# Performance work log

Hardware: AMD Instinct MI355X
Metric: run time of the kernel (lower is better)

Reference implementation:

```python
import jax, jax.numpy as jnp
import numpy as np
from jax import lax


def conv(x, w, b, stride, pad):
    # x: [B,C,H,W], w: [O,I,kh,kw] (torch layout)
    y = lax.conv_general_dilated(x, w, (stride, stride), ((pad, pad), (pad, pad)),
                                 dimension_numbers=('NCHW', 'OIHW', 'NCHW'))
    return y + b[None, :, None, None]


def convT(x, w, b, stride, pad):
    # torch ConvTranspose2d weight layout [in, out, kh, kw]
    k = w.shape[2]
    wf = jnp.flip(w, (2, 3)).transpose(1, 0, 2, 3)  # -> [out, in, kh, kw]
    p = k - 1 - pad
    y = lax.conv_general_dilated(x, wf, (1, 1), ((p, p), (p, p)),
                                 lhs_dilation=(stride, stride),
                                 dimension_numbers=('NCHW', 'OIHW', 'NCHW'))
    return y + b[None, :, None, None]


def resblock(x, wa, ba, wb, bb):
    h = conv(jax.nn.relu(x), wa, ba, 1, 1)   # 3x3
    h2 = conv(jax.nn.relu(h), wb, bb, 1, 0)  # 1x1
    return x + h2


def vqvae_forward(x, e1_w, e1_b, e2_w, e2_b, e3_w, e3_b,
                  er1a_w, er1a_b, er1b_w, er1b_b, er2a_w, er2a_b, er2b_w, er2b_b,
                  codebook,
                  d1_w, d1_b, dr1a_w, dr1a_b, dr1b_w, dr1b_b,
                  dr2a_w, dr2a_b, dr2b_w, dr2b_b,
                  dt1_w, dt1_b, dt2_w, dt2_b):
    # encoder
    h = jax.nn.relu(conv(x, e1_w, e1_b, 2, 1))
    h = jax.nn.relu(conv(h, e2_w, e2_b, 2, 1))
    h = conv(h, e3_w, e3_b, 1, 1)
    h = resblock(h, er1a_w, er1a_b, er1b_w, er1b_b)
    ze = resblock(h, er2a_w, er2a_b, er2b_w, er2b_b)  # [B,C,H,W]
    # VQ: nearest codebook vector per spatial location (squared L2)
    zef = ze.transpose(0, 2, 3, 1)  # [B,H,W,C]
    # ||z - e||^2 = ||z||^2 - 2 z.e + ||e||^2 (same argmin as explicit broadcast)
    d = (jnp.sum(zef * zef, -1, keepdims=True)
         - 2.0 * jnp.einsum('bhwc,kc->bhwk', zef, codebook)
         + jnp.sum(codebook * codebook, -1))  # [B,H,W,K]
    idx = jnp.argmin(d, -1)                    # [B,H,W]
    zq = codebook[idx].transpose(0, 3, 1, 2)   # [B,C,H,W]
    # straight-through estimator
    dec_in = ze + lax.stop_gradient(zq - ze)
    # decoder
    g = conv(dec_in, d1_w, d1_b, 1, 1)
    g = resblock(g, dr1a_w, dr1a_b, dr1b_w, dr1b_b)
    g = resblock(g, dr2a_w, dr2a_b, dr2b_w, dr2b_b)
    g = jax.nn.relu(convT(g, dt1_w, dt1_b, 2, 1))
    x_hat = convT(g, dt2_w, dt2_b, 2, 1)
    return x_hat, ze, zq


def setup_inputs() -> dict:
    key = jax.random.key(0)
    ks = iter(jax.random.split(key, 64))
    C, K = 128, 512

    def w(shape, scale=0.02):
        return jax.random.normal(next(ks), shape, jnp.float32) * scale

    inp = {}
    inp['x'] = jax.random.normal(next(ks), (16, 3, 256, 256), jnp.float32)
    inp['e1_w'] = w((C, 3, 4, 4)); inp['e1_b'] = w((C,))
    inp['e2_w'] = w((C, C, 4, 4)); inp['e2_b'] = w((C,))
    inp['e3_w'] = w((C, C, 3, 3)); inp['e3_b'] = w((C,))
    inp['er1a_w'] = w((C, C, 3, 3)); inp['er1a_b'] = w((C,))
    inp['er1b_w'] = w((C, C, 1, 1)); inp['er1b_b'] = w((C,))
    inp['er2a_w'] = w((C, C, 3, 3)); inp['er2a_b'] = w((C,))
    inp['er2b_w'] = w((C, C, 1, 1)); inp['er2b_b'] = w((C,))
    inp['codebook'] = jax.random.uniform(next(ks), (K, C), jnp.float32, -1.0 / K, 1.0 / K)
    inp['d1_w'] = w((C, C, 3, 3)); inp['d1_b'] = w((C,))
    inp['dr1a_w'] = w((C, C, 3, 3)); inp['dr1a_b'] = w((C,))
    inp['dr1b_w'] = w((C, C, 1, 1)); inp['dr1b_b'] = w((C,))
    inp['dr2a_w'] = w((C, C, 3, 3)); inp['dr2a_b'] = w((C,))
    inp['dr2b_w'] = w((C, C, 1, 1)); inp['dr2b_b'] = w((C,))
    inp['dt1_w'] = w((C, C, 4, 4)); inp['dt1_b'] = w((C,))   # ConvTranspose [in,out,kh,kw]
    inp['dt2_w'] = w((C, 3, 4, 4)); inp['dt2_b'] = w((3,))
    return inp


def reference(x, e1_w, e1_b, e2_w, e2_b, e3_w, e3_b,
              er1a_w, er1a_b, er1b_w, er1b_b, er2a_w, er2a_b, er2b_w, er2b_b,
              codebook,
              d1_w, d1_b, dr1a_w, dr1a_b, dr1b_w, dr1b_b,
              dr2a_w, dr2a_b, dr2b_w, dr2b_b,
              dt1_w, dt1_b, dt2_w, dt2_b):
    return vqvae_forward(x, e1_w, e1_b, e2_w, e2_b, e3_w, e3_b,
                         er1a_w, er1a_b, er1b_w, er1b_b, er2a_w, er2a_b, er2b_w, er2b_b,
                         codebook,
                         d1_w, d1_b, dr1a_w, dr1a_b, dr1b_w, dr1b_b,
                         dr2a_w, dr2a_b, dr2b_w, dr2b_b,
                         dt1_w, dt1_b, dt2_w, dt2_b)
```

## Files before the change

### kernel.cpp

```cpp
#include <hip/hip_runtime.h>
#include <stdint.h>

typedef unsigned short u16;
typedef __attribute__((ext_vector_type(8))) short short8;
typedef __attribute__((ext_vector_type(4))) float floatx4;

#define RS66  (66*128)
#define IS66  (66*66*128)
#define RS130 (130*128)
#define IS130 (130*130*128)

__device__ __forceinline__ float bf2f(u16 h) {
  union { unsigned u; float f; } v; v.u = ((unsigned)h) << 16; return v.f;
}
__device__ __forceinline__ u16 f2bf(float f) {
  union { float f; unsigned u; } v; v.f = f;
  unsigned r = v.u + 0x7FFFu + ((v.u >> 16) & 1u);
  return (u16)(r >> 16);
}
__device__ __forceinline__ unsigned fkey(float f) {
  unsigned u = __float_as_uint(f);
  return (u & 0x80000000u) ? ~u : (u | 0x80000000u);
}
__device__ __forceinline__ void lgkmbar() {
  asm volatile("s_waitcnt lgkmcnt(0)" ::: "memory");
  __builtin_amdgcn_s_barrier();
  __builtin_amdgcn_sched_barrier(0);
}

struct Taps { int n; unsigned dh2; unsigned dw2; };

__global__ __launch_bounds__(256, 3) void conv_mfma(
    const u16* __restrict__ in, int inRS, int inIS, int si,
    const u16* __restrict__ wt, const float* __restrict__ bias, Taps tp,
    u16* __restrict__ out, int outRS, int outIS, int so, int oh0, int ow0,
    const u16* __restrict__ res, u16* __restrict__ out2, int reluMain,
    float* __restrict__ zeFc, u16* __restrict__ zeBFc, int multi)
{
  __shared__ u16 lA[2][8192];
  const int tid = threadIdx.x;
  const int w = tid >> 6, lane = tid & 63, quad = lane >> 4, l16 = lane & 15;
  const int wm = w >> 1, wn = w & 1;
  const int bx = ((blockIdx.x & 7) << 6) | (blockIdx.x >> 3);
  const int blockM = bx << 7;

  unsigned dh2 = tp.dh2, dw2 = tp.dw2;
  if (multi) {
    const int cls = blockIdx.y;
    dh2 = (tp.dh2 >> (8*cls)) & 0xffu;
    dw2 = (tp.dw2 >> (8*cls)) & 0xffu;
    wt += cls << 16;
    oh0 = cls >> 1; ow0 = cls & 1;
  }

  const int swz = (tid & 7) ^ ((tid >> 3) & 7);
  const int wOff = (tid >> 3)*64 + swz*8;
  const u16* gA[4];
#pragma unroll
  for (int i=0;i<4;i++) {
    const int pg = blockM + i*32 + (tid >> 3);
    const int b = pg >> 12, mo = (pg >> 6) & 63, no = pg & 63;
    gA[i] = in + b*inIS + si*mo*inRS + si*no*128 + (tid & 7)*8;
  }
  const u16* gBf = wt + (wn*64 + l16)*32 + quad*8;

  floatx4 zz = {0.f,0.f,0.f,0.f};
  floatx4 acc[4][4];
#pragma unroll
  for (int i=0;i<4;i++)
#pragma unroll
    for (int j=0;j<4;j++) acc[i][j] = zz;

  auto gloadA = [&](int ci, short8 (&a)[4]) {
    const int t = ci >> 1, kc = ci & 1;
    const int dh = (int)((dh2 >> (2*t)) & 3u) - 1;
    const int dw = (int)((dw2 >> (2*t)) & 3u) - 1;
    const int aoff = dh*inRS + dw*128 + kc*64;
#pragma unroll
    for (int i=0;i<4;i++) a[i] = *(const short8*)(gA[i] + aoff);
  };
  auto dswA = [&](u16* P, short8 (&a)[4]) {
#pragma unroll
    for (int i=0;i<4;i++) *(short8*)(P + i*2048 + wOff) = a[i];
  };
  auto loadBk = [&](int ci, int kk, short8 (&v)[4]) {
    const u16* p = gBf + ci*8192 + kk*4096;
#pragma unroll
    for (int s=0;s<4;s++) v[s] = *(const short8*)(p + s*512);
  };
  auto computeH = [&](const u16* P, int kk, short8 (&bfr)[4]) {
    short8 af[4];
#pragma unroll
    for (int s=0;s<4;s++) {
      const int row = wm*64 + s*16 + l16;
      af[s] = *(const short8*)&P[row*64 + (((kk*4 + quad) ^ (l16 & 7)) << 3)];
    }
#pragma unroll
    for (int i=0;i<4;i++)
#pragma unroll
      for (int j=0;j<4;j++)
        acc[i][j] = __builtin_amdgcn_mfma_f32_16x16x32_bf16(af[i], bfr[j], acc[i][j], 0, 0, 0);
  };

  const int NCH = tp.n << 1;
  short8 a[4], bA[4], bB[4];
  gloadA(0, a);
  loadBk(0, 0, bA);
  loadBk(0, 1, bB);
  dswA(&lA[0][0], a);
  gloadA(1, a);
  lgkmbar();

  int cur = 0;
  for (int ci = 0; ci < NCH; ++ci) {
    computeH(&lA[cur][0], 0, bA);
    if (ci + 1 < NCH) loadBk(ci + 1, 0, bA);
    computeH(&lA[cur][0], 1, bB);
    if (ci + 1 < NCH) {
      loadBk(ci + 1, 1, bB);
      dswA(&lA[cur ^ 1][0], a);
      if (ci + 2 < NCH) gloadA(ci + 2, a);
      lgkmbar();
    }
    cur ^= 1;
  }

  float bv[4];
#pragma unroll
  for (int j=0;j<4;j++) bv[j] = bias[wn*64 + j*16 + l16];

#pragma unroll
  for (int i=0;i<4;i++) {
#pragma unroll
    for (int r=0;r<4;r++) {
      const int p = blockM + wm*64 + i*16 + quad*4 + r;
      const int bb2 = p >> 12, mo = (p >> 6) & 63, no = p & 63;
      const int ob = bb2*outIS + (so*mo + oh0)*outRS + (so*no + ow0)*128;
#pragma unroll
      for (int j=0;j<4;j++) {
        const int n = wn*64 + j*16 + l16;
        float v = acc[i][j][r] + bv[j];
        if (res)  v += bf2f(res[ob + n]);
        if (out)  out[ob + n]  = f2bf(reluMain ? fmaxf(v, 0.f) : v);
        if (out2) out2[ob + n] = f2bf(fmaxf(v, 0.f));
        if (zeFc) {
          zeFc[((size_t)p << 7) + n] = v;
          zeBFc[((size_t)p << 7) + n] = f2bf(v);
        }
      }
    }
  }
}

__global__ __launch_bounds__(256, 3) void vq_score(
    const u16* __restrict__ zeBF, const u16* __restrict__ cbF,
    const float* __restrict__ cbn, unsigned long long* __restrict__ minbuf)
{
  __shared__ u16 lA[2][8192];
  const int tid = threadIdx.x;
  const int w = tid >> 6, lane = tid & 63, quad = lane >> 4, l16 = lane & 15;
  const int wm = w >> 1, wn = w & 1;
  const int bx = ((blockIdx.x & 7) << 6) | (blockIdx.x >> 3);
  const int blockM = bx << 7;
  const int nb = blockIdx.y;
  const int swz = (tid & 7) ^ ((tid >> 3) & 7);
  const int wOff = (tid >> 3)*64 + swz*8;
  const u16* gA[4];
#pragma unroll
  for (int i=0;i<4;i++)
    gA[i] = zeBF + ((size_t)(blockM + i*32 + (tid >> 3)) << 7) + (tid & 7)*8;
  const u16* gBf = cbF + (nb << 14) + (wn*64 + l16)*32 + quad*8;

  floatx4 zz = {0.f,0.f,0.f,0.f};
  floatx4 acc[4][4];
#pragma unroll
  for (int i=0;i<4;i++)
#pragma unroll
    for (int j=0;j<4;j++) acc[i][j] = zz;

  auto gloadA = [&](int ci, short8 (&a)[4]) {
#pragma unroll
    for (int i=0;i<4;i++) a[i] = *(const short8*)(gA[i] + ci*64);
  };
  auto dswA = [&](u16* P, short8 (&a)[4]) {
#pragma unroll
    for (int i=0;i<4;i++) *(short8*)(P + i*2048 + wOff) = a[i];
  };
  auto loadBk = [&](int ci, int kk, short8 (&v)[4]) {
    const u16* p = gBf + ci*8192 + kk*4096;
#pragma unroll
    for (int s=0;s<4;s++) v[s] = *(const short8*)(p + s*512);
  };
  auto computeH = [&](const u16* P, int kk, short8 (&bfr)[4]) {
    short8 af[4];
#pragma unroll
    for (int s=0;s<4;s++) {
      const int row = wm*64 + s*16 + l16;
      af[s] = *(const short8*)&P[row*64 + (((kk*4 + quad) ^ (l16 & 7)) << 3)];
    }
#pragma unroll
    for (int i=0;i<4;i++)
#pragma unroll
      for (int j=0;j<4;j++)
        acc[i][j] = __builtin_amdgcn_mfma_f32_16x16x32_bf16(af[i], bfr[j], acc[i][j], 0, 0, 0);
  };

  short8 a[4], bA[4], bB[4];
  gloadA(0, a);
  loadBk(0, 0, bA);
  loadBk(0, 1, bB);
  dswA(&lA[0][0], a);
  gloadA(1, a);
  lgkmbar();
  computeH(&lA[0][0], 0, bA);
  loadBk(1, 0, bA);
  computeH(&lA[0][0], 1, bB);
  loadBk(1, 1, bB);
  dswA(&lA[1][0], a);
  lgkmbar();
  computeH(&lA[1][0], 0, bA);
  computeH(&lA[1][0], 1, bB);

  float cn[4];
#pragma unroll
  for (int j=0;j<4;j++) cn[j] = cbn[nb*128 + wn*64 + j*16 + l16];

#pragma unroll
  for (int i=0;i<4;i++) {
#pragma unroll
    for (int r=0;r<4;r++) {
      const int p = blockM + wm*64 + i*16 + quad*4 + r;
      unsigned long long best = 0xFFFFFFFFFFFFFFFFull;
#pragma unroll
      for (int j=0;j<4;j++) {
        const int n = nb*128 + wn*64 + j*16 + l16;
        float v = cn[j] - acc[i][j][r];
        unsigned long long pk = ((unsigned long long)fkey(v) << 32) | (unsigned)n;
        if (pk < best) best = pk;
      }
#pragma unroll
      for (int d=1; d<16; d<<=1) {
        unsigned long long o = __shfl_xor(best, d, 64);
        if (o < best) best = o;
      }
      if (l16 == 0) atomicMin(minbuf + p, best);
    }
  }
}

__global__ __launch_bounds__(256) void finalize(
    const float* __restrict__ zeFc, const unsigned long long* __restrict__ minb,
    const float* __restrict__ cb, float* __restrict__ outZe, float* __restrict__ outZq,
    u16* __restrict__ zqI)
{
  __shared__ float T[64*129];
  __shared__ int ns[64];
  const int tid = threadIdx.x;
  const int P0 = blockIdx.x << 6;
  const int b = P0 >> 12, hw0 = P0 & 4095;

#pragma unroll
  for (int it=0; it<32; ++it) {
    int e = it*256 + tid;
    int px = e >> 7, c = e & 127;
    T[px*129 + c] = zeFc[((size_t)P0 << 7) + e];
  }
  if (tid < 64) ns[tid] = (int)(unsigned)(minb[P0 + tid] & 0xFFFFFFFFull);
  __syncthreads();

  float* zeB = outZe + (((size_t)b) << 19) + hw0;
  float* zqB = outZq + (((size_t)b) << 19) + hw0;
  const int h = hw0 >> 6;
  u16* zqIB = zqI + b*IS66 + h*RS66;
#pragma unroll
  for (int it=0; it<32; ++it) {
    const int c = it*4 + (tid >> 6);
    const int px = tid & 63;
    zeB[(c << 12) + px] = T[px*129 + c];
    float v = cb[(ns[px] << 7) + c];
    zqB[(c << 12) + px] = v;
    zqIB[px*128 + c] = f2bf(v);
  }
}

__global__ __launch_bounds__(256) void zero_halos(
    u16* big, u16* s0, u16* s1, u16* s2, u16* s3, unsigned long long* minb)
{
  int id = blockIdx.x*256 + threadIdx.x;
  if (id >= 463872) return;
  if (id >= 398336) { minb[id - 398336] = 0xFFFFFFFFFFFFFFFFull; return; }
  u16* base; int H, W;
  if (id < 132096) { base = big; H = 128; W = 128; }
  else {
    id -= 132096;
    int bi = id / 66560;
    id -= bi*66560;
    base = (bi == 0) ? s0 : (bi == 1) ? s1 : (bi == 2) ? s2 : s3;
    H = 64; W = 64;
  }
  int Wp = W+2, Hp = H+2;
  int cv = id & 15; int rest = id >> 4;
  int npx = 2*Wp + 2*H;
  int img = rest / npx; int pix = rest - img*npx;
  int hh, wwp;
  if (pix < Wp) { hh = 0; wwp = pix; }
  else if (pix < 2*Wp) { hh = Hp-1; wwp = pix - Wp; }
  else { int r2 = pix - 2*Wp; hh = 1 + (r2 >> 1); wwp = (r2 & 1) ? (Wp-1) : 0; }
  uint4 zv = {0u,0u,0u,0u};
  *(uint4*)(base + (((size_t)img*Hp + hh)*Wp + wwp)*128 + cv*8) = zv;
}

struct WEnt { const float* src; u16* dst; int O, I, T, mode; };
struct WTab { int n; WEnt e[16]; int cum[17]; };
__global__ __launch_bounds__(256) void prep_w(WTab wt) {
  int id = blockIdx.x*256 + threadIdx.x;
  if (id >= wt.cum[wt.n]) return;
  int k = 0;
  while (id >= wt.cum[k+1]) k++;
  int l = id - wt.cum[k];
  WEnt E = wt.e[k];
  if (E.mode == 6) {
    int e = l & 7, quad = (l >> 3) & 3, row = (l >> 5) & 127;
    int kk = (l >> 12) & 1, kc = (l >> 13) & 1, t = l >> 14;
    int i = kc*64 + kk*32 + quad*8 + e;
    E.dst[l] = f2bf(E.src[(row*E.I + i)*E.T + t]);
  } else if (E.mode == 1) {
    int e = l & 7, quad = (l >> 3) & 3, row = (l >> 5) & 127;
    int kk = (l >> 12) & 1, kc = (l >> 13) & 1, tt = (l >> 14) & 3, cls = l >> 16;
    int i = kc*64 + kk*32 + quad*8 + e;
    int th = tt >> 1, tw = tt & 1, po = cls >> 1, pw = cls & 1;
    int kh = po ? (th ? 2 : 0) : (th ? 3 : 1);
    int kw = pw ? (tw ? 2 : 0) : (tw ? 3 : 1);
    E.dst[l] = f2bf(E.src[((i*128 + row)*4 + kh)*4 + kw]);
  } else if (E.mode == 7) {
    int e = l & 7, quad = (l >> 3) & 3, row = (l >> 5) & 127;
    int kk = (l >> 12) & 1, kc = (l >> 13) & 1, tt = l >> 14;
    int i = kc*64 + kk*32 + quad*8 + e;
    E.dst[l] = f2bf(E.src[(tt*128 + row)*128 + i]);
  } else if (E.mode == 3) {
    float s = 0.f; const float* r = E.src + l*128;
    for (int c=0;c<128;c++) s += r[c]*r[c];
    ((float*)E.dst)[l] = 0.5f*s;
  } else if (E.mode == 4) {
    int o = l & 127, tap = l >> 7;
    ((float*)E.dst)[l] = E.src[o*48 + tap];
  } else {
    int c = l & 127, n = l >> 7;
    int o = n >> 4, kk = n & 15;
    E.dst[l] = f2bf(E.src[c*48 + o*16 + kk]);
  }
}

__global__ __launch_bounds__(256) void conv_e1(
    const float* __restrict__ x, const float* __restrict__ wT,
    const float* __restrict__ bias, u16* __restrict__ outI)
{
  __shared__ float inS[12*260];
  __shared__ float wS[48*128];
  __shared__ float bS[128];
  const int tid = threadIdx.x;
  const int b = blockIdx.x >> 7, ho = blockIdx.x & 127;

  for (int l = tid; l < 1536; l += 256)
    ((float4*)wS)[l] = ((const float4*)wT)[l];
  if (tid < 128) bS[tid] = bias[tid];
  for (int l = tid; l < 3120; l += 256) {
    int col = l % 260; int rest = l / 260;
    int kh = rest & 3, c = rest >> 2;
    int hi = 2*ho + kh - 1, wi = col - 1;
    float v = 0.f;
    if ((unsigned)hi < 256u && (unsigned)wi < 256u)
      v = x[((b*3 + c) << 16) + (hi << 8) + wi];
    inS[rest*260 + col] = v;
  }
  __syncthreads();

  const int g = tid & 7;
  const int pxg = tid >> 3;
  floatx4 acc[4][4];
  {
    const floatx4* bp = (const floatx4*)&bS[g*16];
    floatx4 b0 = bp[0], b1 = bp[1], b2 = bp[2], b3 = bp[3];
#pragma unroll
    for (int px=0;px<4;px++) { acc[px][0]=b0; acc[px][1]=b1; acc[px][2]=b2; acc[px][3]=b3; }
  }
#pragma unroll
  for (int c=0;c<3;c++)
#pragma unroll
    for (int kh=0;kh<4;kh++) {
      const float* row = &inS[(c*4+kh)*260];
#pragma unroll
      for (int kw=0;kw<4;kw++) {
        const int tap = c*16 + kh*4 + kw;
        const floatx4* wp = (const floatx4*)&wS[tap*128 + g*16];
        floatx4 w0 = wp[0], w1 = wp[1], w2 = wp[2], w3 = wp[3];
#pragma unroll
        for (int px=0;px<4;px++) {
          float xv = row[((pxg*4 + px) << 1) + kw];
          acc[px][0] += xv*w0; acc[px][1] += xv*w1;
          acc[px][2] += xv*w2; acc[px][3] += xv*w3;
        }
      }
    }

  u16* ob = outI + b*IS130 + ho*RS130;
#pragma unroll
  for (int px=0;px<4;px++) {
    const int wo = pxg*4 + px;
    u16* p = ob + wo*128 + g*16;
#pragma unroll
    for (int k=0;k<4;k++) {
      union { u16 u[4]; uint2 v2; } pk;
#pragma unroll
      for (int j=0;j<4;j++) pk.u[j] = f2bf(fmaxf(acc[px][k][j], 0.f));
      *(uint2*)(p + k*4) = pk.v2;
    }
  }
}

__global__ __launch_bounds__(256) void dt2_gemm(
    const u16* __restrict__ inI, const u16* __restrict__ Wb,
    float* __restrict__ cols)
{
  const int tid = threadIdx.x;
  const int w = tid >> 6, lane = tid & 63, quad = lane >> 4, l16 = lane & 15;
  const int pixBase = blockIdx.x*256 + w*64;

  short8 Bf[3][4];
#pragma unroll
  for (int nt=0; nt<3; nt++)
#pragma unroll
    for (int kc=0; kc<4; kc++)
      Bf[nt][kc] = *(const short8*)(Wb + (nt*16 + l16)*128 + kc*32 + quad*8);

  const u16* ap[4];
#pragma unroll
  for (int ms=0; ms<4; ms++) {
    int p = pixBase + ms*16 + l16;
    int b = p >> 14, rem = p & 16383;
    ap[ms] = inI + b*IS130 + (rem >> 7)*RS130 + (rem & 127)*128;
  }

  floatx4 zz = {0.f,0.f,0.f,0.f};
  floatx4 acc[4][3];
#pragma unroll
  for (int ms=0; ms<4; ms++)
#pragma unroll
    for (int nt=0; nt<3; nt++) acc[ms][nt] = zz;

#pragma unroll
  for (int kc=0; kc<4; kc++) {
#pragma unroll
    for (int ms=0; ms<4; ms++) {
      short8 a = *(const short8*)(ap[ms] + kc*32 + quad*8);
#pragma unroll
      for (int nt=0; nt<3; nt++)
        acc[ms][nt] = __builtin_amdgcn_mfma_f32_16x16x32_bf16(a, Bf[nt][kc], acc[ms][nt], 0, 0, 0);
    }
  }

#pragma unroll
  for (int ms=0; ms<4; ms++)
#pragma unroll
    for (int nt=0; nt<3; nt++)
#pragma unroll
      for (int r=0; r<4; r++) {
        int p = pixBase + ms*16 + quad*4 + r;
        cols[(size_t)p*48 + nt*16 + l16] = acc[ms][nt][r];
      }
}

__global__ __launch_bounds__(256) void dt2_gather(
    const float* __restrict__ cols, const float* __restrict__ bias,
    float* __restrict__ xhat)
{
  int id = blockIdx.x*256 + threadIdx.x;
  int b = id >> 16, rem = id & 65535;
  int ho = rem >> 8, wo = rem & 255;
  const int ph = ho & 1, pw = wo & 1;
  const int hi0 = ph ? ((ho+1)>>1) : (ho>>1);
  const int kh0 = ph ? 0 : 1;
  const int wi0 = pw ? ((wo+1)>>1) : (wo>>1);
  const int kw0 = pw ? 0 : 1;
  float a0 = bias[0], a1 = bias[1], a2 = bias[2];
#pragma unroll
  for (int th=0; th<2; th++) {
    const int hi = hi0 - th;
    if ((unsigned)hi >= 128u) continue;
    const int kh = kh0 + 2*th;
#pragma unroll
    for (int tw=0; tw<2; tw++) {
      const int wi = wi0 - tw;
      if ((unsigned)wi >= 128u) continue;
      const int kw = kw0 + 2*tw;
      const float* r = cols + (size_t)((b << 14) + (hi << 7) + wi)*48 + (kh*4 + kw);
      a0 += r[0]; a1 += r[16]; a2 += r[32];
    }
  }
  const int ob = ((b*3) << 16) + (ho << 8) + wo;
  xhat[ob]          = a0;
  xhat[ob + 65536]  = a1;
  xhat[ob + 131072] = a2;
}

extern "C" void kernel_launch(void* const* d_in, const int* in_sizes, int n_in,
                              void* d_out, int out_size, void* d_ws, size_t ws_size,
                              hipStream_t stream)
{
  const float* x     = (const float*)d_in[0];
  const float* e1w   = (const float*)d_in[1];
  const float* e1b   = (const float*)d_in[2];
  const float* e2w   = (const float*)d_in[3];
  const float* e2b   = (const float*)d_in[4];
  const float* e3w   = (const float*)d_in[5];
  const float* e3b   = (const float*)d_in[6];
  const float* er1aw = (const float*)d_in[7];
  const float* er1ab = (const float*)d_in[8];
  const float* er1bw = (const float*)d_in[9];
  const float* er1bb = (const float*)d_in[10];
  const float* er2aw = (const float*)d_in[11];
  const float* er2ab = (const float*)d_in[12];
  const float* er2bw = (const float*)d_in[13];
  const float* er2bb = (const float*)d_in[14];
  const float* cb    = (const float*)d_in[15];
  const float* d1w   = (const float*)d_in[16];
  const float* d1b   = (const float*)d_in[17];
  const float* dr1aw = (const float*)d_in[18];
  const float* dr1ab = (const float*)d_in[19];
  const float* dr1bw = (const float*)d_in[20];
  const float* dr1bb = (const float*)d_in[21];
  const float* dr2aw = (const float*)d_in[22];
  const float* dr2ab = (const float*)d_in[23];
  const float* dr2bw = (const float*)d_in[24];
  const float* dr2bb = (const float*)d_in[25];
  const float* dt1w  = (const float*)d_in[26];
  const float* dt1b  = (const float*)d_in[27];
  const float* dt2w  = (const float*)d_in[28];
  const float* dt2b  = (const float*)d_in[29];
  float* out = (float*)d_out;

  char* ws = (char*)d_ws;
  size_t off = 0;
  auto alloc = [&](size_t bytes) -> void* {
    void* r = ws + off; off += (bytes + 255) & ~(size_t)255; return r;
  };

  u16* BIG = (u16*)alloc((size_t)IS130*16*2);
  u16* S[4];
  for (int i=0;i<4;i++) S[i] = (u16*)alloc((size_t)IS66*16*2);
  unsigned long long* minb = (unsigned long long*)alloc((size_t)65536*8);
  u16* W_e2 = (u16*)alloc(262144*2);
  u16* W9[6]; for (int i=0;i<6;i++) W9[i] = (u16*)alloc(147456*2);
  u16* W1[4]; for (int i=0;i<4;i++) W1[i] = (u16*)alloc(16384*2);
  u16* Wdt1 = (u16*)alloc(262144*2);
  u16* cbBF = (u16*)alloc(65536*2);
  float* cbn = (float*)alloc(512*4);
  float* wsE1 = (float*)alloc(6144*4);
  u16* Wb48 = (u16*)alloc(6144*2);

  u16* BIGi = BIG + RS130 + 128;
  u16* Si[4];
  for (int i=0;i<4;i++) Si[i] = S[i] + RS66 + 128;
  u16* zeBFc = S[1];
  float* zeFc = (float*)BIG;
  float* cols = (float*)S[1];

  zero_halos<<<1812, 256, 0, stream>>>(BIG, S[0], S[1], S[2], S[3], minb);

  WTab wtab; int ne = 0; wtab.cum[0] = 0;
  auto addw = [&](const float* s, u16* d, int O, int I, int T, int m, int items) {
    wtab.e[ne] = {s, d, O, I, T, m};
    wtab.cum[ne+1] = wtab.cum[ne] + items; ne++;
  };
  addw(e2w,   W_e2, 128,128,16,6, 262144);
  addw(e3w,   W9[0],128,128, 9,6, 147456);
  addw(er1aw, W9[1],128,128, 9,6, 147456);
  addw(er2aw, W9[2],128,128, 9,6, 147456);
  addw(d1w,   W9[3],128,128, 9,6, 147456);
  addw(dr1aw, W9[4],128,128, 9,6, 147456);
  addw(dr2aw, W9[5],128,128, 9,6, 147456);
  addw(er1bw, W1[0],128,128, 1,6, 16384);
  addw(er2bw, W1[1],128,128, 1,6, 16384);
  addw(dr1bw, W1[2],128,128, 1,6, 16384);
  addw(dr2bw, W1[3],128,128, 1,6, 16384);
  addw(dt1w,  Wdt1, 0,0,0,1, 262144);
  addw(cb,    cbBF, 0,0,0,7, 65536);
  addw(cb,    (u16*)cbn, 0,0,0,3, 512);
  addw(e1w,   (u16*)wsE1, 0,0,0,4, 6144);
  addw(dt2w,  Wb48, 0,0,0,5, 6144);
  wtab.n = ne;
  prep_w<<<(wtab.cum[ne] + 255)/256, 256, 0, stream>>>(wtab);

  conv_e1<<<2048, 256, 0, stream>>>(x, wsE1, e1b, BIGi);

  Taps t16; t16.n = 16; t16.dh2 = 0; t16.dw2 = 0;
  for (int t=0;t<16;t++) { t16.dh2 |= (unsigned)(t>>2) << (2*t); t16.dw2 |= (unsigned)(t&3) << (2*t); }
  Taps t9; t9.n = 9; t9.dh2 = 0; t9.dw2 = 0;
  for (int t=0;t<9;t++) { t9.dh2 |= (unsigned)(t/3) << (2*t); t9.dw2 |= (unsigned)(t%3) << (2*t); }
  Taps t1x; t1x.n = 1; t1x.dh2 = 1; t1x.dw2 = 1;
  Taps tcm; tcm.n = 4; tcm.dh2 = 0; tcm.dw2 = 0;
  for (int cls=0; cls<4; ++cls) {
    int po = cls >> 1, pw = cls & 1;
    for (int tt=0; tt<4; ++tt) {
      int th = tt >> 1, tw = tt & 1;
      int dh = po ? (th ? 0 : 1) : (th ? -1 : 0);
      int dw = pw ? (tw ? 0 : 1) : (tw ? -1 : 0);
      tcm.dh2 |= (unsigned)(dh+1) << (8*cls + 2*tt);
      tcm.dw2 |= (unsigned)(dw+1) << (8*cls + 2*tt);
    }
  }

  auto conv = [&](const u16* in_, int iRS, int iIS, int si,
                  const u16* w_, const float* b_, Taps tp,
                  u16* o_, int oRS, int oIS, int so, int oh, int ow,
                  const u16* r_, u16* o2, int rl, float* zf, u16* zb) {
    conv_mfma<<<512, 256, 0, stream>>>(in_, iRS, iIS, si, w_, b_, tp,
                                       o_, oRS, oIS, so, oh, ow, r_, o2, rl, zf, zb, 0);
  };

  conv(BIGi, RS130, IS130, 2, W_e2, e2b, t16, Si[0], RS66, IS66, 1,0,0, nullptr, nullptr, 1, nullptr, nullptr);
  conv(Si[0], RS66, IS66, 1, W9[0], e3b, t9, Si[1], RS66, IS66, 1,0,0, nullptr, Si[2], 0, nullptr, nullptr);
  conv(Si[2], RS66, IS66, 1, W9[1], er1ab, t9, Si[0], RS66, IS66, 1,0,0, nullptr, nullptr, 1, nullptr, nullptr);
  conv(Si[0], RS66, IS66, 1, W1[0], er1bb, t1x, Si[3], RS66, IS66, 1,0,0, Si[1], Si[2], 0, nullptr, nullptr);
  conv(Si[2], RS66, IS66, 1, W9[2], er2ab, t9, Si[0], RS66, IS66, 1,0,0, nullptr, nullptr, 1, nullptr, nullptr);
  conv(Si[0], RS66, IS66, 1, W1[1], er2bb, t1x, nullptr, RS66, IS66, 1,0,0, Si[3], nullptr, 0, zeFc, zeBFc);

  vq_score<<<dim3(512,4), 256, 0, stream>>>(zeBFc, cbBF, cbn, minb);
  finalize<<<1024, 256, 0, stream>>>(zeFc, minb, cb, out + 3145728, out + 11534336, Si[2]);

  conv(Si[2], RS66, IS66, 1, W9[3], d1b, t9, Si[0], RS66, IS66, 1,0,0, nullptr, Si[1], 0, nullptr, nullptr);
  conv(Si[1], RS66, IS66, 1, W9[4], dr1ab, t9, Si[2], RS66, IS66, 1,0,0, nullptr, nullptr, 1, nullptr, nullptr);
  conv(Si[2], RS66, IS66, 1, W1[2], dr1bb, t1x, Si[3], RS66, IS66, 1,0,0, Si[0], Si[1], 0, nullptr, nullptr);
  conv(Si[1], RS66, IS66, 1, W9[5], dr2ab, t9, Si[2], RS66, IS66, 1,0,0, nullptr, nullptr, 1, nullptr, nullptr);
  conv(Si[2], RS66, IS66, 1, W1[3], dr2bb, t1x, Si[0], RS66, IS66, 1,0,0, Si[3], nullptr, 0, nullptr, nullptr);

  conv_mfma<<<dim3(512,4), 256, 0, stream>>>(Si[0], RS66, IS66, 1, Wdt1, dt1b, tcm,
                                             BIGi, RS130, IS130, 2, 0, 0,
                                             nullptr, nullptr, 1, nullptr, nullptr, 1);

  dt2_gemm<<<1024, 256, 0, stream>>>(BIGi, Wb48, cols);
  dt2_gather<<<4096, 256, 0, stream>>>(cols, dt2b, out);
}
```

Before: 726.4 us.

## Widen conv and VQ GEMM K-chunk to full 128 channels per tap

Each K-step in the MFMA conv and VQ scoring kernels now stages a full 128-channel tap (128x128 bf16 A tile) in LDS instead of two 64-channel halves. This halves the number of barriers and LDS double-buffer swaps per tap. The B fragments are loaded in four sub-steps interleaved with compute, and the weight prep layout is changed to match. It doubles LDS use and register use for A staging, so launch bounds drop from 3 to 2 blocks per CU, which lowers occupancy.

```diff
diff --git a/kernel.cpp b/kernel.cpp
--- a/kernel.cpp
+++ b/kernel.cpp
@@ -30,14 +30,14 @@
 
 struct Taps { int n; unsigned dh2; unsigned dw2; };
 
-__global__ __launch_bounds__(256, 3) void conv_mfma(
+__global__ __launch_bounds__(256, 2) void conv_mfma(
     const u16* __restrict__ in, int inRS, int inIS, int si,
     const u16* __restrict__ wt, const float* __restrict__ bias, Taps tp,
     u16* __restrict__ out, int outRS, int outIS, int so, int oh0, int ow0,
     const u16* __restrict__ res, u16* __restrict__ out2, int reluMain,
     float* __restrict__ zeFc, u16* __restrict__ zeBFc, int multi)
 {
-  __shared__ u16 lA[2][8192];
+  __shared__ u16 lA[2][16384];
   const int tid = threadIdx.x;
   const int w = tid >> 6, lane = tid & 63, quad = lane >> 4, l16 = lane & 15;
   const int wm = w >> 1, wn = w & 1;
@@ -53,8 +53,8 @@
     oh0 = cls >> 1; ow0 = cls & 1;
   }
 
-  const int swz = (tid & 7) ^ ((tid >> 3) & 7);
-  const int wOff = (tid >> 3)*64 + swz*8;
+  const int swz3 = (tid & 7) ^ ((tid >> 3) & 7);
+  const int wBase = (tid >> 3)*128 + swz3*8;
   const u16* gA[4];
 #pragma unroll
   for (int i=0;i<4;i++) {
@@ -71,29 +71,34 @@
 #pragma unroll
     for (int j=0;j<4;j++) acc[i][j] = zz;
 
-  auto gloadA = [&](int ci, short8 (&a)[4]) {
-    const int t = ci >> 1, kc = ci & 1;
+  auto gloadA = [&](int t, short8 (&a)[8]) {
     const int dh = (int)((dh2 >> (2*t)) & 3u) - 1;
     const int dw = (int)((dw2 >> (2*t)) & 3u) - 1;
-    const int aoff = dh*inRS + dw*128 + kc*64;
-#pragma unroll
-    for (int i=0;i<4;i++) a[i] = *(const short8*)(gA[i] + aoff);
-  };
-  auto dswA = [&](u16* P, short8 (&a)[4]) {
-#pragma unroll
-    for (int i=0;i<4;i++) *(short8*)(P + i*2048 + wOff) = a[i];
+    const int aoff = dh*inRS + dw*128;
+#pragma unroll
+    for (int i=0;i<4;i++)
+#pragma unroll
+      for (int h=0;h<2;h++)
+        a[i*2+h] = *(const short8*)(gA[i] + aoff + h*64);
+  };
+  auto dswA = [&](u16* P, short8 (&a)[8]) {
+#pragma unroll
+    for (int i=0;i<4;i++)
+#pragma unroll
+      for (int h=0;h<2;h++)
+        *(short8*)(P + i*4096 + wBase + h*64) = a[i*2+h];
   };
   auto loadBk = [&](int ci, int kk, short8 (&v)[4]) {
-    const u16* p = gBf + ci*8192 + kk*4096;
-#pragma unroll
-    for (int s=0;s<4;s++) v[s] = *(const short8*)(p + s*512);
+    const u16* p = gBf + ci*16384 + kk*4096;
+#pragma unroll
+    for (int s4=0;s4<4;s4++) v[s4] = *(const short8*)(p + s4*512);
   };
   auto computeH = [&](const u16* P, int kk, short8 (&bfr)[4]) {
     short8 af[4];
 #pragma unroll
-    for (int s=0;s<4;s++) {
-      const int row = wm*64 + s*16 + l16;
-      af[s] = *(const short8*)&P[row*64 + (((kk*4 + quad) ^ (l16 & 7)) << 3)];
+    for (int s4=0;s4<4;s4++) {
+      const int row = wm*64 + s4*16 + l16;
+      af[s4] = *(const short8*)&P[row*128 + (((kk*4 + quad) ^ (l16 & 7)) << 3)];
     }
 #pragma unroll
     for (int i=0;i<4;i++)
@@ -102,26 +107,29 @@
         acc[i][j] = __builtin_amdgcn_mfma_f32_16x16x32_bf16(af[i], bfr[j], acc[i][j], 0, 0, 0);
   };
 
-  const int NCH = tp.n << 1;
-  short8 a[4], bA[4], bB[4];
+  const int NCH = tp.n;
+  short8 a[8], bA[4], bB[4];
   gloadA(0, a);
   loadBk(0, 0, bA);
-  loadBk(0, 1, bB);
   dswA(&lA[0][0], a);
-  gloadA(1, a);
+  if (NCH > 1) gloadA(1, a);
   lgkmbar();
 
   int cur = 0;
   for (int ci = 0; ci < NCH; ++ci) {
+    loadBk(ci, 1, bB);
     computeH(&lA[cur][0], 0, bA);
-    if (ci + 1 < NCH) loadBk(ci + 1, 0, bA);
+    loadBk(ci, 2, bA);
     computeH(&lA[cur][0], 1, bB);
+    loadBk(ci, 3, bB);
+    computeH(&lA[cur][0], 2, bA);
     if (ci + 1 < NCH) {
-      loadBk(ci + 1, 1, bB);
+      loadBk(ci + 1, 0, bA);
       dswA(&lA[cur ^ 1][0], a);
       if (ci + 2 < NCH) gloadA(ci + 2, a);
-      lgkmbar();
-    }
+    }
+    computeH(&lA[cur][0], 3, bB);
+    if (ci + 1 < NCH) lgkmbar();
     cur ^= 1;
   }
 
@@ -152,19 +160,19 @@
   }
 }
 
-__global__ __launch_bounds__(256, 3) void vq_score(
+__global__ __launch_bounds__(256, 2) void vq_score(
     const u16* __restrict__ zeBF, const u16* __restrict__ cbF,
     const float* __restrict__ cbn, unsigned long long* __restrict__ minbuf)
 {
-  __shared__ u16 lA[2][8192];
+  __shared__ u16 lA[16384];
   const int tid = threadIdx.x;
   const int w = tid >> 6, lane = tid & 63, quad = lane >> 4, l16 = lane & 15;
   const int wm = w >> 1, wn = w & 1;
   const int bx = ((blockIdx.x & 7) << 6) | (blockIdx.x >> 3);
   const int blockM = bx << 7;
   const int nb = blockIdx.y;
-  const int swz = (tid & 7) ^ ((tid >> 3) & 7);
-  const int wOff = (tid >> 3)*64 + swz*8;
+  const int swz3 = (tid & 7) ^ ((tid >> 3) & 7);
+  const int wBase = (tid >> 3)*128 + swz3*8;
   const u16* gA[4];
 #pragma unroll
   for (int i=0;i<4;i++)
@@ -178,25 +186,17 @@
 #pragma unroll
     for (int j=0;j<4;j++) acc[i][j] = zz;
 
-  auto gloadA = [&](int ci, short8 (&a)[4]) {
-#pragma unroll
-    for (int i=0;i<4;i++) a[i] = *(const short8*)(gA[i] + ci*64);
-  };
-  auto dswA = [&](u16* P, short8 (&a)[4]) {
-#pragma unroll
-    for (int i=0;i<4;i++) *(short8*)(P + i*2048 + wOff) = a[i];
-  };
-  auto loadBk = [&](int ci, int kk, short8 (&v)[4]) {
-    const u16* p = gBf + ci*8192 + kk*4096;
-#pragma unroll
-    for (int s=0;s<4;s++) v[s] = *(const short8*)(p + s*512);
-  };
-  auto computeH = [&](const u16* P, int kk, short8 (&bfr)[4]) {
+  auto loadBk = [&](int kk, short8 (&v)[4]) {
+    const u16* p = gBf + kk*4096;
+#pragma unroll
+    for (int s4=0;s4<4;s4++) v[s4] = *(const short8*)(p + s4*512);
+  };
+  auto computeH = [&](int kk, short8 (&bfr)[4]) {
     short8 af[4];
 #pragma unroll
-    for (int s=0;s<4;s++) {
-      const int row = wm*64 + s*16 + l16;
-      af[s] = *(const short8*)&P[row*64 + (((kk*4 + quad) ^ (l16 & 7)) << 3)];
+    for (int s4=0;s4<4;s4++) {
+      const int row = wm*64 + s4*16 + l16;
+      af[s4] = *(const short8*)&lA[row*128 + (((kk*4 + quad) ^ (l16 & 7)) << 3)];
     }
 #pragma unroll
     for (int i=0;i<4;i++)
@@ -205,21 +205,26 @@
         acc[i][j] = __builtin_amdgcn_mfma_f32_16x16x32_bf16(af[i], bfr[j], acc[i][j], 0, 0, 0);
   };
 
-  short8 a[4], bA[4], bB[4];
-  gloadA(0, a);
-  loadBk(0, 0, bA);
-  loadBk(0, 1, bB);
-  dswA(&lA[0][0], a);
-  gloadA(1, a);
+  short8 a[8], bA[4], bB[4];
+#pragma unroll
+  for (int i=0;i<4;i++)
+#pragma unroll
+    for (int h=0;h<2;h++)
+      a[i*2+h] = *(const short8*)(gA[i] + h*64);
+  loadBk(0, bA);
+#pragma unroll
+  for (int i=0;i<4;i++)
+#pragma unroll
+    for (int h=0;h<2;h++)
+      *(short8*)(lA + i*4096 + wBase + h*64) = a[i*2+h];
   lgkmbar();
-  computeH(&lA[0][0], 0, bA);
-  loadBk(1, 0, bA);
-  computeH(&lA[0][0], 1, bB);
-  loadBk(1, 1, bB);
-  dswA(&lA[1][0], a);
-  lgkmbar();
-  computeH(&lA[1][0], 0, bA);
-  computeH(&lA[1][0], 1, bB);
+  loadBk(1, bB);
+  computeH(0, bA);
+  loadBk(2, bA);
+  computeH(1, bB);
+  loadBk(3, bB);
+  computeH(2, bA);
+  computeH(3, bB);
 
   float cn[4];
 #pragma unroll
@@ -321,21 +326,21 @@
   WEnt E = wt.e[k];
   if (E.mode == 6) {
     int e = l & 7, quad = (l >> 3) & 3, row = (l >> 5) & 127;
-    int kk = (l >> 12) & 1, kc = (l >> 13) & 1, t = l >> 14;
-    int i = kc*64 + kk*32 + quad*8 + e;
+    int kk = (l >> 12) & 3, t = l >> 14;
+    int i = kk*32 + quad*8 + e;
     E.dst[l] = f2bf(E.src[(row*E.I + i)*E.T + t]);
   } else if (E.mode == 1) {
     int e = l & 7, quad = (l >> 3) & 3, row = (l >> 5) & 127;
-    int kk = (l >> 12) & 1, kc = (l >> 13) & 1, tt = (l >> 14) & 3, cls = l >> 16;
-    int i = kc*64 + kk*32 + quad*8 + e;
+    int kk = (l >> 12) & 3, tt = (l >> 14) & 3, cls = l >> 16;
+    int i = kk*32 + quad*8 + e;
     int th = tt >> 1, tw = tt & 1, po = cls >> 1, pw = cls & 1;
     int kh = po ? (th ? 2 : 0) : (th ? 3 : 1);
     int kw = pw ? (tw ? 2 : 0) : (tw ? 3 : 1);
     E.dst[l] = f2bf(E.src[((i*128 + row)*4 + kh)*4 + kw]);
   } else if (E.mode == 7) {
     int e = l & 7, quad = (l >> 3) & 3, row = (l >> 5) & 127;
-    int kk = (l >> 12) & 1, kc = (l >> 13) & 1, tt = l >> 14;
-    int i = kc*64 + kk*32 + quad*8 + e;
+    int kk = (l >> 12) & 3, tt = l >> 14;
+    int i = kk*32 + quad*8 + e;
     E.dst[l] = f2bf(E.src[(tt*128 + row)*128 + i]);
   } else if (E.mode == 3) {
     float s = 0.f; const float* r = E.src + l*128;
```

Result: slower. 782.8 us (+7.8%).
